# Kernel optimization log

Hardware: AMD Instinct MI355X
Metric: run time of the kernel (lower is better)

The kernel has to match this reference:

```python
import jax, jax.numpy as jnp
import numpy as np

B, C_IN, L = 4, 512, 16384
C_RED = C_IN // 2  # q/k/v reduced channels = 256
BL = 64            # sliding-window block size
NEG = -jnp.inf


def setup_inputs() -> dict:
    key = jax.random.key(0)
    ks = jax.random.split(key, 8)
    x1 = jax.random.normal(ks[0], (B, C_IN, L), dtype=jnp.float32)
    x2 = jax.random.normal(ks[1], (B, C_IN, L), dtype=jnp.float32)
    mask = jnp.ones((B, 1, L), dtype=jnp.float32)
    s = 0.02
    Wq = jax.random.normal(ks[2], (C_RED, C_IN), dtype=jnp.float32) * s
    Wk = jax.random.normal(ks[3], (C_RED, C_IN), dtype=jnp.float32) * s
    Wv = jax.random.normal(ks[4], (C_RED, C_IN), dtype=jnp.float32) * s
    Wo = jax.random.normal(ks[5], (C_IN, C_RED), dtype=jnp.float32) * s
    bq = jnp.zeros((C_RED,), jnp.float32)
    bk = jnp.zeros((C_RED,), jnp.float32)
    bv = jnp.zeros((C_RED,), jnp.float32)
    bo = jnp.zeros((C_IN,), jnp.float32)
    return {"x1": x1, "x2": x2, "mask": mask, "Wq": Wq, "bq": bq,
            "Wk": Wk, "bk": bk, "Wv": Wv, "bv": bv, "Wo": Wo, "bo": bo}


def _conv1x1(W, b, x):
    # x: (B, Cin, L) -> (B, Cout, L)
    return jnp.einsum('oc,bcl->bol', W, x) + b[None, :, None]


def reference(x1, x2, mask, Wq, bq, Wk, bk, Wv, bv, Wo, bo):
    # encoder stage: value comes from x1 (x2 unused)
    q = _conv1x1(Wq, bq, x1)  # (B, C, L)
    k = _conv1x1(Wk, bk, x1)
    v = _conv1x1(Wv, bv, x1)

    Bq, C, Lq = q.shape
    bl = BL
    nb = (Lq + bl - 1) // bl
    pad = nb * bl - Lq
    if pad > 0:
        q = jnp.pad(q, ((0, 0), (0, 0), (0, pad)))
        k = jnp.pad(k, ((0, 0), (0, 0), (0, pad)))
        v = jnp.pad(v, ((0, 0), (0, 0), (0, pad)))
        mask = jnp.pad(mask, ((0, 0), (0, 0), (0, pad)))

    # non-overlapping windows: (B, C, nb, bl)
    qb = q.reshape(Bq, C, nb, bl)
    kb = k.reshape(Bq, C, nb, bl)
    vb = v.reshape(Bq, C, nb, bl)
    mb = mask.reshape(Bq, 1, nb, bl)  # (B,1,nb,bl)

    scale = 1.0 / jnp.sqrt(jnp.float32(C))
    # per-block attention scores: (B, nb, bl_i, bl_j)
    scores = jnp.einsum('bcni,bcnj->bnij', qb, kb) * scale
    key_mask = mb[:, 0, :, None, :]  # (B, nb, 1, bl_j)
    scores = jnp.where(key_mask == 0, NEG, scores)
    probs = jax.nn.softmax(scores, axis=-1)
    attn = jnp.einsum('bnij,bcnj->bcni', probs, vb)  # (B, C, nb, bl)

    h = jax.nn.relu(attn)
    out = jnp.einsum('oc,bcni->boni', Wo, h) + bo[None, :, None, None]
    out = out.reshape(Bq, Wo.shape[0], nb * bl)
    if pad > 0:
        out = out[:, :, :Lq]
    return out
```

## Files before the change

### kernel.cpp

```cpp
#include <hip/hip_runtime.h>
#include <hip/hip_fp16.h>
#include <stdint.h>

#define BB    4
#define CIN   512
#define CRED  256
#define LL    16384
#define NBLK  256
#define WELEM 131072

typedef _Float16 half8 __attribute__((ext_vector_type(8)));
typedef float    f32x4 __attribute__((ext_vector_type(4)));

#define XT_OFF 0
#define Q_OFF  0
#define K_OFF  32768
#define V_OFF  32768
#define H_OFF  0
#define P_OFF  65536
#define MSK_OFF 73728
#define LDS_BYTES 73984

#define SWZ(r) (((r)&7)<<4)

__global__ void convert_weights(const float* __restrict__ Wq,
                                const float* __restrict__ Wk,
                                const float* __restrict__ Wv,
                                const float* __restrict__ Wo,
                                _Float16* __restrict__ dst) {
    int i = blockIdx.x * blockDim.x + threadIdx.x;
    int m = i >> 17;
    int e = i & (WELEM - 1);
    const float* src = (m == 0) ? Wq : (m == 1) ? Wk : (m == 2) ? Wv : Wo;
    dst[(size_t)m * WELEM + e] = (_Float16)src[e];
}

__global__ __launch_bounds__(256, 2)
void att_fused(const float* __restrict__ x1, const float* __restrict__ mask,
               const _Float16* __restrict__ W,
               const float* __restrict__ bq, const float* __restrict__ bk,
               const float* __restrict__ bv, const float* __restrict__ bo,
               float* __restrict__ out) {
    extern __shared__ char lds[];
    const int tid  = threadIdx.x;
    const int wid  = tid >> 6;
    const int lane = tid & 63;
    const int l15  = lane & 15;
    const int l4   = lane >> 4;
    const int blk  = blockIdx.x;
    const int b    = blk >> 8;
    const int n    = blk & 255;
    const int jx   = tid & 15;
    const int rb   = tid >> 4;

    const _Float16* Wq = W;
    const _Float16* Wk = W + WELEM;
    const _Float16* Wv = W + 2 * WELEM;
    const _Float16* Wo = W + 3 * WELEM;

    {
        const float* xbase = x1 + ((size_t)b * CIN + 2 * rb) * LL + n * 64 + 4 * jx;
        #pragma unroll
        for (int i = 0; i < 16; ++i) {
            f32x4 a = *(const f32x4*)(xbase + (size_t)(32 * i) * LL);
            f32x4 c = *(const f32x4*)(xbase + (size_t)(32 * i + 1) * LL);
            const int col = 4 * rb + 64 * i;
            #pragma unroll
            for (int u = 0; u < 4; ++u) {
                union { _Float16 h[2]; uint32_t w; } p;
                p.h[0] = (_Float16)a[u];
                p.h[1] = (_Float16)c[u];
                const int j = 4 * jx + u;
                *(uint32_t*)(lds + XT_OFF + j * 1024 + (col ^ SWZ(j))) = p.w;
            }
        }
        if (tid < 64)
            *(float*)(lds + MSK_OFF + tid * 4) = mask[(size_t)b * LL + n * 64 + tid];
    }
    __syncthreads();

    uint64_t qh[4][4], kh[4][4], vh[4][4];
    #pragma unroll
    for (int pass = 0; pass < 4; ++pass) {
        f32x4 aQ[4], aK[4], aV[4];
        #pragma unroll
        for (int q = 0; q < 4; ++q) {
            aQ[q] = (f32x4){0.f, 0.f, 0.f, 0.f};
            aK[q] = (f32x4){0.f, 0.f, 0.f, 0.f};
            aV[q] = (f32x4){0.f, 0.f, 0.f, 0.f};
        }
        const int mrow = wid * 64 + pass * 16 + l15;
        const _Float16* wqp = Wq + (size_t)mrow * CIN + l4 * 8;
        const _Float16* wkp = Wk + (size_t)mrow * CIN + l4 * 8;
        const _Float16* wvp = Wv + (size_t)mrow * CIN + l4 * 8;
        #pragma unroll 4
        for (int ks = 0; ks < 16; ++ks) {
            const int kb = ks * 64 + l4 * 16;
            half8 xb[4];
            #pragma unroll
            for (int nt = 0; nt < 4; ++nt) {
                const int j = nt * 16 + l15;
                xb[nt] = *(const half8*)(lds + XT_OFF + j * 1024 + (kb ^ SWZ(j)));
            }
            half8 aq = *(const half8*)(wqp + ks * 32);
            half8 ak = *(const half8*)(wkp + ks * 32);
            half8 av = *(const half8*)(wvp + ks * 32);
            #pragma unroll
            for (int nt = 0; nt < 4; ++nt) {
                aQ[nt] = __builtin_amdgcn_mfma_f32_16x16x32_f16(aq, xb[nt], aQ[nt], 0, 0, 0);
                aK[nt] = __builtin_amdgcn_mfma_f32_16x16x32_f16(ak, xb[nt], aK[nt], 0, 0, 0);
                aV[nt] = __builtin_amdgcn_mfma_f32_16x16x32_f16(av, xb[nt], aV[nt], 0, 0, 0);
            }
        }
        const int c0 = wid * 64 + pass * 16 + l4 * 4;
        f32x4 bqv = *(const f32x4*)(bq + c0);
        f32x4 bkv = *(const f32x4*)(bk + c0);
        f32x4 bvv = *(const f32x4*)(bv + c0);
        #pragma unroll
        for (int nt = 0; nt < 4; ++nt) {
            union { _Float16 h[4]; uint64_t q; } qp, kp, vp;
            #pragma unroll
            for (int ri = 0; ri < 4; ++ri) {
                qp.h[ri] = (_Float16)(aQ[nt][ri] + bqv[ri]);
                kp.h[ri] = (_Float16)(aK[nt][ri] + bkv[ri]);
                vp.h[ri] = (_Float16)(aV[nt][ri] + bvv[ri]);
            }
            qh[pass][nt] = qp.q;
            kh[pass][nt] = kp.q;
            vh[pass][nt] = vp.q;
        }
    }
    __syncthreads();

    #pragma unroll
    for (int pass = 0; pass < 4; ++pass) {
        const int c0 = wid * 64 + pass * 16 + l4 * 4;
        #pragma unroll
        for (int nt = 0; nt < 4; ++nt) {
            const int j = nt * 16 + l15;
            *(uint64_t*)(lds + Q_OFF + j * 512 + ((2 * c0) ^ SWZ(j))) = qh[pass][nt];
            *(uint64_t*)(lds + K_OFF + j * 512 + ((2 * c0) ^ SWZ(j))) = kh[pass][nt];
        }
    }
    __syncthreads();

    {
        const int i0 = wid * 16;
        f32x4 sa[4];
        #pragma unroll
        for (int jt = 0; jt < 4; ++jt) sa[jt] = (f32x4){0.f, 0.f, 0.f, 0.f};
        #pragma unroll
        for (int ks = 0; ks < 8; ++ks) {
            const int kb = ks * 64 + l4 * 16;
            const int iq = i0 + l15;
            half8 qa = *(const half8*)(lds + Q_OFF + iq * 512 + (kb ^ SWZ(iq)));
            #pragma unroll
            for (int jt = 0; jt < 4; ++jt) {
                const int jr = jt * 16 + l15;
                half8 kf = *(const half8*)(lds + K_OFF + jr * 512 + (kb ^ SWZ(jr)));
                sa[jt] = __builtin_amdgcn_mfma_f32_16x16x32_f16(qa, kf, sa[jt], 0, 0, 0);
            }
        }
        float msk[4];
        #pragma unroll
        for (int jt = 0; jt < 4; ++jt)
            msk[jt] = *(const float*)(lds + MSK_OFF + (jt * 16 + l15) * 4);
        #pragma unroll
        for (int ri = 0; ri < 4; ++ri) {
            float v[4];
            #pragma unroll
            for (int jt = 0; jt < 4; ++jt)
                v[jt] = (msk[jt] == 0.f) ? -1e30f : sa[jt][ri] * 0.0625f;
            float mx = fmaxf(fmaxf(v[0], v[1]), fmaxf(v[2], v[3]));
            mx = fmaxf(mx, __shfl_xor(mx, 1));
            mx = fmaxf(mx, __shfl_xor(mx, 2));
            mx = fmaxf(mx, __shfl_xor(mx, 4));
            mx = fmaxf(mx, __shfl_xor(mx, 8));
            float e[4], sum = 0.f;
            #pragma unroll
            for (int jt = 0; jt < 4; ++jt) { e[jt] = __expf(v[jt] - mx); sum += e[jt]; }
            sum += __shfl_xor(sum, 1);
            sum += __shfl_xor(sum, 2);
            sum += __shfl_xor(sum, 4);
            sum += __shfl_xor(sum, 8);
            const float inv = 1.f / sum;
            const int i = i0 + l4 * 4 + ri;
            #pragma unroll
            for (int jt = 0; jt < 4; ++jt) {
                const int j = jt * 16 + l15;
                *(_Float16*)(lds + P_OFF + i * 128 + ((2 * j) ^ SWZ(i))) =
                    (_Float16)(e[jt] * inv);
            }
        }
    }
    __syncthreads();

    #pragma unroll
    for (int pass = 0; pass < 4; ++pass) {
        const int c0 = wid * 64 + pass * 16 + l4 * 4;
        #pragma unroll
        for (int nt = 0; nt < 4; ++nt) {
            const int j = nt * 16 + l15;
            const uint64_t v64 = vh[pass][nt];
            #pragma unroll
            for (int ri = 0; ri < 4; ++ri) {
                const int c = c0 + ri;
                *(uint16_t*)(lds + V_OFF + c * 128 + ((2 * j) ^ SWZ(c))) =
                    (uint16_t)(v64 >> (16 * ri));
            }
        }
    }
    __syncthreads();

    {
        const int cb = wid * 64;
        f32x4 pv[4][4];
        #pragma unroll
        for (int m = 0; m < 4; ++m)
            #pragma unroll
            for (int q = 0; q < 4; ++q) pv[m][q] = (f32x4){0.f, 0.f, 0.f, 0.f};
        #pragma unroll
        for (int ks = 0; ks < 2; ++ks) {
            const int kb = ks * 64 + l4 * 16;
            half8 pb[4];
            #pragma unroll
            for (int nt = 0; nt < 4; ++nt) {
                const int i = nt * 16 + l15;
                pb[nt] = *(const half8*)(lds + P_OFF + i * 128 + (kb ^ SWZ(i)));
            }
            #pragma unroll
            for (int mt = 0; mt < 4; ++mt) {
                const int c = cb + mt * 16 + l15;
                half8 va = *(const half8*)(lds + V_OFF + c * 128 + (kb ^ SWZ(c)));
                #pragma unroll
                for (int nt = 0; nt < 4; ++nt)
                    pv[mt][nt] = __builtin_amdgcn_mfma_f32_16x16x32_f16(va, pb[nt], pv[mt][nt], 0, 0, 0);
            }
        }
        #pragma unroll
        for (int mt = 0; mt < 4; ++mt) {
            const int c0 = cb + mt * 16 + l4 * 4;
            #pragma unroll
            for (int nt = 0; nt < 4; ++nt) {
                const int j = nt * 16 + l15;
                union { _Float16 h[4]; uint64_t q; } hp;
                #pragma unroll
                for (int ri = 0; ri < 4; ++ri)
                    hp.h[ri] = (_Float16)fmaxf(pv[mt][nt][ri], 0.f);
                *(uint64_t*)(lds + H_OFF + j * 512 + ((2 * c0) ^ SWZ(j))) = hp.q;
            }
        }
    }
    __syncthreads();

    #pragma unroll
    for (int op = 0; op < 2; ++op) {
        const int mbo = wid * 128 + op * 64;
        const _Float16* wob = Wo + (size_t)(mbo + l15) * CRED + l4 * 8;
        f32x4 oa[4][4];
        #pragma unroll
        for (int m = 0; m < 4; ++m)
            #pragma unroll
            for (int q = 0; q < 4; ++q) oa[m][q] = (f32x4){0.f, 0.f, 0.f, 0.f};
        #pragma unroll 4
        for (int ks = 0; ks < 8; ++ks) {
            const int kb = ks * 64 + l4 * 16;
            half8 hb[4];
            #pragma unroll
            for (int nt = 0; nt < 4; ++nt) {
                const int i = nt * 16 + l15;
                hb[nt] = *(const half8*)(lds + H_OFF + i * 512 + (kb ^ SWZ(i)));
            }
            #pragma unroll
            for (int mt = 0; mt < 4; ++mt) {
                half8 wa = *(const half8*)(wob + mt * 16 * CRED + ks * 32);
                #pragma unroll
                for (int nt = 0; nt < 4; ++nt)
                    oa[mt][nt] = __builtin_amdgcn_mfma_f32_16x16x32_f16(wa, hb[nt], oa[mt][nt], 0, 0, 0);
            }
        }
        #pragma unroll
        for (int mt = 0; mt < 4; ++mt) {
            const int o0 = mbo + mt * 16 + l4 * 4;
            f32x4 bov = *(const f32x4*)(bo + o0);
            #pragma unroll
            for (int ri = 0; ri < 4; ++ri) {
                float* orow = out + ((size_t)b * CIN + (o0 + ri)) * LL + n * 64;
                #pragma unroll
                for (int nt = 0; nt < 4; ++nt)
                    orow[nt * 16 + l15] = oa[mt][nt][ri] + bov[ri];
            }
        }
    }
}

extern "C" void kernel_launch(void* const* d_in, const int* in_sizes, int n_in,
                              void* d_out, int out_size, void* d_ws, size_t ws_size,
                              hipStream_t stream) {
    const float* x1   = (const float*)d_in[0];
    const float* mask = (const float*)d_in[2];
    const float* Wq   = (const float*)d_in[3];
    const float* bq   = (const float*)d_in[4];
    const float* Wk   = (const float*)d_in[5];
    const float* bk   = (const float*)d_in[6];
    const float* Wv   = (const float*)d_in[7];
    const float* bv   = (const float*)d_in[8];
    const float* Wo   = (const float*)d_in[9];
    const float* bo   = (const float*)d_in[10];
    float* out = (float*)d_out;
    _Float16* wbuf = (_Float16*)d_ws;

    (void)hipFuncSetAttribute((const void*)att_fused,
                              hipFuncAttributeMaxDynamicSharedMemorySize, LDS_BYTES);

    convert_weights<<<2048, 256, 0, stream>>>(Wq, Wk, Wv, Wo, wbuf);
    att_fused<<<BB * NBLK, 256, LDS_BYTES, stream>>>(x1, mask, wbuf, bq, bk, bv, bo, out);
}
```

Baseline: 167.9 us.

## Hoist LDS X reads across QKV passes and vectorize x1 staging stores

The QKV projection loop is restructured so each K-step loads the four X fragments from LDS once and reuses them for all four 16-row passes. All 48 accumulators are kept live instead of 12. The x1 staging now reads 8 channel rows per thread and writes packed half8 LDS stores instead of 32-bit stores. This cuts LDS read traffic and store count, but raises VGPR/AGPR pressure a lot (192 accumulator floats), which may cause spills or lower occupancy under launch_bounds(256,2).

```diff
diff --git a/kernel.cpp b/kernel.cpp
--- a/kernel.cpp
+++ b/kernel.cpp
@@ -50,8 +50,6 @@
     const int blk  = blockIdx.x;
     const int b    = blk >> 8;
     const int n    = blk & 255;
-    const int jx   = tid & 15;
-    const int rb   = tid >> 4;
 
     const _Float16* Wq = W;
     const _Float16* Wk = W + WELEM;
@@ -59,19 +57,22 @@
     const _Float16* Wo = W + 3 * WELEM;
 
     {
-        const float* xbase = x1 + ((size_t)b * CIN + 2 * rb) * LL + n * 64 + 4 * jx;
-        #pragma unroll
-        for (int i = 0; i < 16; ++i) {
-            f32x4 a = *(const f32x4*)(xbase + (size_t)(32 * i) * LL);
-            f32x4 c = *(const f32x4*)(xbase + (size_t)(32 * i + 1) * LL);
-            const int col = 4 * rb + 64 * i;
+        const int jx = tid & 15;
+        const int rg = tid >> 4;
+        const float* xp = x1 + ((size_t)b * CIN + 8 * rg) * LL + n * 64 + 4 * jx;
+        #pragma unroll
+        for (int i = 0; i < 4; ++i) {
+            f32x4 r[8];
+            #pragma unroll
+            for (int r8 = 0; r8 < 8; ++r8)
+                r[r8] = *(const f32x4*)(xp + (size_t)(128 * i + r8) * LL);
             #pragma unroll
             for (int u = 0; u < 4; ++u) {
-                union { _Float16 h[2]; uint32_t w; } p;
-                p.h[0] = (_Float16)a[u];
-                p.h[1] = (_Float16)c[u];
                 const int j = 4 * jx + u;
-                *(uint32_t*)(lds + XT_OFF + j * 1024 + (col ^ SWZ(j))) = p.w;
+                union { _Float16 h[8]; half8 v; } pk;
+                #pragma unroll
+                for (int r8 = 0; r8 < 8; ++r8) pk.h[r8] = (_Float16)r[r8][u];
+                *(half8*)(lds + XT_OFF + j * 1024 + ((16 * rg + 256 * i) ^ SWZ(j))) = pk.v;
             }
         }
         if (tid < 64)
@@ -79,20 +80,19 @@
     }
     __syncthreads();
 
-    uint64_t qh[4][4], kh[4][4], vh[4][4];
+    f32x4 aQ[4][4], aK[4][4], aV[4][4];
     #pragma unroll
-    for (int pass = 0; pass < 4; ++pass) {
-        f32x4 aQ[4], aK[4], aV[4];
+    for (int p = 0; p < 4; ++p)
         #pragma unroll
         for (int q = 0; q < 4; ++q) {
-            aQ[q] = (f32x4){0.f, 0.f, 0.f, 0.f};
-            aK[q] = (f32x4){0.f, 0.f, 0.f, 0.f};
-            aV[q] = (f32x4){0.f, 0.f, 0.f, 0.f};
-        }
-        const int mrow = wid * 64 + pass * 16 + l15;
-        const _Float16* wqp = Wq + (size_t)mrow * CIN + l4 * 8;
-        const _Float16* wkp = Wk + (size_t)mrow * CIN + l4 * 8;
-        const _Float16* wvp = Wv + (size_t)mrow * CIN + l4 * 8;
+            aQ[p][q] = (f32x4){0.f, 0.f, 0.f, 0.f};
+            aK[p][q] = (f32x4){0.f, 0.f, 0.f, 0.f};
+            aV[p][q] = (f32x4){0.f, 0.f, 0.f, 0.f};
+        }
+    {
+        const _Float16* wq0 = Wq + (size_t)(wid * 64 + l15) * CIN + l4 * 8;
+        const _Float16* wk0 = Wk + (size_t)(wid * 64 + l15) * CIN + l4 * 8;
+        const _Float16* wv0 = Wv + (size_t)(wid * 64 + l15) * CIN + l4 * 8;
         #pragma unroll 4
         for (int ks = 0; ks < 16; ++ks) {
             const int kb = ks * 64 + l4 * 16;
@@ -102,44 +102,43 @@
                 const int j = nt * 16 + l15;
                 xb[nt] = *(const half8*)(lds + XT_OFF + j * 1024 + (kb ^ SWZ(j)));
             }
-            half8 aq = *(const half8*)(wqp + ks * 32);
-            half8 ak = *(const half8*)(wkp + ks * 32);
-            half8 av = *(const half8*)(wvp + ks * 32);
-            #pragma unroll
-            for (int nt = 0; nt < 4; ++nt) {
-                aQ[nt] = __builtin_amdgcn_mfma_f32_16x16x32_f16(aq, xb[nt], aQ[nt], 0, 0, 0);
-                aK[nt] = __builtin_amdgcn_mfma_f32_16x16x32_f16(ak, xb[nt], aK[nt], 0, 0, 0);
-                aV[nt] = __builtin_amdgcn_mfma_f32_16x16x32_f16(av, xb[nt], aV[nt], 0, 0, 0);
-            }
-        }
+            #pragma unroll
+            for (int pass = 0; pass < 4; ++pass) {
+                const size_t wo = (size_t)pass * 16 * CIN + ks * 32;
+                half8 aq = *(const half8*)(wq0 + wo);
+                half8 ak = *(const half8*)(wk0 + wo);
+                half8 av = *(const half8*)(wv0 + wo);
+                #pragma unroll
+                for (int nt = 0; nt < 4; ++nt) {
+                    aQ[pass][nt] = __builtin_amdgcn_mfma_f32_16x16x32_f16(aq, xb[nt], aQ[pass][nt], 0, 0, 0);
+                    aK[pass][nt] = __builtin_amdgcn_mfma_f32_16x16x32_f16(ak, xb[nt], aK[pass][nt], 0, 0, 0);
+                    aV[pass][nt] = __builtin_amdgcn_mfma_f32_16x16x32_f16(av, xb[nt], aV[pass][nt], 0, 0, 0);
+                }
+            }
+        }
+    }
+    __syncthreads();
+
+    uint64_t vh[4][4];
+    #pragma unroll
+    for (int pass = 0; pass < 4; ++pass) {
         const int c0 = wid * 64 + pass * 16 + l4 * 4;
         f32x4 bqv = *(const f32x4*)(bq + c0);
         f32x4 bkv = *(const f32x4*)(bk + c0);
         f32x4 bvv = *(const f32x4*)(bv + c0);
         #pragma unroll
         for (int nt = 0; nt < 4; ++nt) {
+            const int j = nt * 16 + l15;
             union { _Float16 h[4]; uint64_t q; } qp, kp, vp;
             #pragma unroll
             for (int ri = 0; ri < 4; ++ri) {
-                qp.h[ri] = (_Float16)(aQ[nt][ri] + bqv[ri]);
-                kp.h[ri] = (_Float16)(aK[nt][ri] + bkv[ri]);
-                vp.h[ri] = (_Float16)(aV[nt][ri] + bvv[ri]);
-            }
-            qh[pass][nt] = qp.q;
-            kh[pass][nt] = kp.q;
+                qp.h[ri] = (_Float16)(aQ[pass][nt][ri] + bqv[ri]);
+                kp.h[ri] = (_Float16)(aK[pass][nt][ri] + bkv[ri]);
+                vp.h[ri] = (_Float16)(aV[pass][nt][ri] + bvv[ri]);
+            }
+            *(uint64_t*)(lds + Q_OFF + j * 512 + ((2 * c0) ^ SWZ(j))) = qp.q;
+            *(uint64_t*)(lds + K_OFF + j * 512 + ((2 * c0) ^ SWZ(j))) = kp.q;
             vh[pass][nt] = vp.q;
-        }
-    }
-    __syncthreads();
-
-    #pragma unroll
-    for (int pass = 0; pass < 4; ++pass) {
-        const int c0 = wid * 64 + pass * 16 + l4 * 4;
-        #pragma unroll
-        for (int nt = 0; nt < 4; ++nt) {
-            const int j = nt * 16 + l15;
-            *(uint64_t*)(lds + Q_OFF + j * 512 + ((2 * c0) ^ SWZ(j))) = qh[pass][nt];
-            *(uint64_t*)(lds + K_OFF + j * 512 + ((2 * c0) ^ SWZ(j))) = kh[pass][nt];
         }
     }
     __syncthreads();
```

After: 291.4 us. 1.74x slower.

## Split fused attention kernel into QKV GEMM and attention/output kernels via workspace

Applied to the files above, without the earlier changes.

Replaces the single fused kernel with two kernels when the workspace is large enough. The first computes Q, K and V in fp16 and writes them to global workspace. The second reads them back and runs masked softmax, PV, ReLU and the output projection using less LDS, which allows higher occupancy (3 blocks per CU). This trades extra global traffic (about 100MB of fp16 writes and reads) for lower LDS pressure and more occupancy in each stage. The old fused kernel remains as a fallback.

```diff
diff --git a/kernel.cpp b/kernel.cpp
--- a/kernel.cpp
+++ b/kernel.cpp
@@ -12,16 +12,12 @@
 typedef _Float16 half8 __attribute__((ext_vector_type(8)));
 typedef float    f32x4 __attribute__((ext_vector_type(4)));
 
-#define XT_OFF 0
-#define Q_OFF  0
-#define K_OFF  32768
-#define V_OFF  32768
-#define H_OFF  0
-#define P_OFF  65536
-#define MSK_OFF 73728
-#define LDS_BYTES 73984
-
 #define SWZ(r) (((r)&7)<<4)
+
+#define QBASE   524288
+#define TILE_E  16384
+#define MAT_E   16777216
+#define WS_NEED ((size_t)(QBASE + 3 * MAT_E) * 2)
 
 __global__ void convert_weights(const float* __restrict__ Wq,
                                 const float* __restrict__ Wk,
@@ -34,6 +30,260 @@
     const float* src = (m == 0) ? Wq : (m == 1) ? Wk : (m == 2) ? Wv : Wo;
     dst[(size_t)m * WELEM + e] = (_Float16)src[e];
 }
+
+__global__ __launch_bounds__(256, 2)
+void qkv_gemm(const float* __restrict__ x1, const _Float16* __restrict__ W,
+              const float* __restrict__ bq, const float* __restrict__ bk,
+              const float* __restrict__ bv, _Float16* __restrict__ ws) {
+    extern __shared__ char lds[];
+    const int tid = threadIdx.x;
+    const int wid = tid >> 6;
+    const int l15 = tid & 15;
+    const int l4  = (tid & 63) >> 4;
+    const int b   = blockIdx.x >> 8;
+    const int n   = blockIdx.x & 255;
+
+    {
+        const int jx = tid & 15;
+        const int rg = tid >> 4;
+        const float* xp = x1 + ((size_t)b * CIN + 8 * rg) * LL + n * 64 + 4 * jx;
+        #pragma unroll
+        for (int i = 0; i < 4; ++i) {
+            f32x4 r[8];
+            #pragma unroll
+            for (int r8 = 0; r8 < 8; ++r8)
+                r[r8] = *(const f32x4*)(xp + (size_t)(128 * i + r8) * LL);
+            #pragma unroll
+            for (int u = 0; u < 4; ++u) {
+                const int j = 4 * jx + u;
+                union { _Float16 h[8]; half8 v; } pk;
+                #pragma unroll
+                for (int r8 = 0; r8 < 8; ++r8) pk.h[r8] = (_Float16)r[r8][u];
+                *(half8*)(lds + j * 1024 + ((16 * rg + 256 * i) ^ SWZ(j))) = pk.v;
+            }
+        }
+    }
+    __syncthreads();
+
+    const size_t t = (size_t)blockIdx.x * TILE_E;
+    #pragma unroll
+    for (int p = 0; p < 3; ++p) {
+        f32x4 am[4][4];
+        #pragma unroll
+        for (int m = 0; m < 4; ++m)
+            #pragma unroll
+            for (int q = 0; q < 4; ++q) am[m][q] = (f32x4){0.f, 0.f, 0.f, 0.f};
+        const _Float16* wp = W + (size_t)p * WELEM + (size_t)(wid * 64 + l15) * CIN + l4 * 8;
+        #pragma unroll 4
+        for (int ks = 0; ks < 16; ++ks) {
+            const int kb = ks * 64 + l4 * 16;
+            half8 xb[4];
+            #pragma unroll
+            for (int nt = 0; nt < 4; ++nt) {
+                const int j = nt * 16 + l15;
+                xb[nt] = *(const half8*)(lds + j * 1024 + (kb ^ SWZ(j)));
+            }
+            #pragma unroll
+            for (int mt = 0; mt < 4; ++mt) {
+                half8 wf = *(const half8*)(wp + mt * 16 * CIN + ks * 32);
+                #pragma unroll
+                for (int nt = 0; nt < 4; ++nt)
+                    am[mt][nt] = __builtin_amdgcn_mfma_f32_16x16x32_f16(wf, xb[nt], am[mt][nt], 0, 0, 0);
+            }
+        }
+        const float* bias = (p == 0) ? bq : (p == 1) ? bk : bv;
+        if (p < 2) {
+            _Float16* dst = ws + QBASE + (size_t)p * MAT_E + t;
+            #pragma unroll
+            for (int mt = 0; mt < 4; ++mt) {
+                const int c0 = wid * 64 + mt * 16 + l4 * 4;
+                f32x4 b4 = *(const f32x4*)(bias + c0);
+                #pragma unroll
+                for (int nt = 0; nt < 4; ++nt) {
+                    const int j = nt * 16 + l15;
+                    union { _Float16 h[4]; uint64_t q; } pk;
+                    #pragma unroll
+                    for (int ri = 0; ri < 4; ++ri)
+                        pk.h[ri] = (_Float16)(am[mt][nt][ri] + b4[ri]);
+                    *(uint64_t*)(dst + (size_t)j * 256 + c0) = pk.q;
+                }
+            }
+        } else {
+            _Float16* dst = ws + QBASE + 2 * (size_t)MAT_E + t;
+            #pragma unroll
+            for (int mt = 0; mt < 4; ++mt) {
+                const int c0 = wid * 64 + mt * 16 + l4 * 4;
+                f32x4 b4 = *(const f32x4*)(bias + c0);
+                #pragma unroll
+                for (int nt = 0; nt < 4; ++nt) {
+                    const int j = nt * 16 + l15;
+                    #pragma unroll
+                    for (int ri = 0; ri < 4; ++ri)
+                        dst[(size_t)(c0 + ri) * 64 + j] = (_Float16)(am[mt][nt][ri] + b4[ri]);
+                }
+            }
+        }
+    }
+}
+
+#define BH_OFF 0
+#define BP_OFF 32768
+#define LDS_B  40960
+
+__global__ __launch_bounds__(256, 3)
+void attn_out(const float* __restrict__ mask, const _Float16* __restrict__ ws,
+              const float* __restrict__ bo, float* __restrict__ out) {
+    extern __shared__ char lds[];
+    const int tid = threadIdx.x;
+    const int wid = tid >> 6;
+    const int l15 = tid & 15;
+    const int l4  = (tid & 63) >> 4;
+    const int b   = blockIdx.x >> 8;
+    const int n   = blockIdx.x & 255;
+
+    const size_t t = (size_t)blockIdx.x * TILE_E;
+    const _Float16* qt = ws + QBASE + t;
+    const _Float16* kt = qt + MAT_E;
+    const _Float16* vt = qt + 2 * (size_t)MAT_E;
+    const _Float16* Wo = ws + 3 * (size_t)WELEM;
+
+    {
+        const int i0 = wid * 16;
+        f32x4 sa[4];
+        #pragma unroll
+        for (int jt = 0; jt < 4; ++jt) sa[jt] = (f32x4){0.f, 0.f, 0.f, 0.f};
+        #pragma unroll
+        for (int ks = 0; ks < 8; ++ks) {
+            half8 qa = *(const half8*)(qt + (size_t)(i0 + l15) * 256 + ks * 32 + l4 * 8);
+            #pragma unroll
+            for (int jt = 0; jt < 4; ++jt) {
+                half8 kf = *(const half8*)(kt + (size_t)(jt * 16 + l15) * 256 + ks * 32 + l4 * 8);
+                sa[jt] = __builtin_amdgcn_mfma_f32_16x16x32_f16(qa, kf, sa[jt], 0, 0, 0);
+            }
+        }
+        float msk[4];
+        #pragma unroll
+        for (int jt = 0; jt < 4; ++jt)
+            msk[jt] = mask[(size_t)b * LL + n * 64 + jt * 16 + l15];
+        #pragma unroll
+        for (int ri = 0; ri < 4; ++ri) {
+            float v[4];
+            #pragma unroll
+            for (int jt = 0; jt < 4; ++jt)
+                v[jt] = (msk[jt] == 0.f) ? -1e30f : sa[jt][ri] * 0.0625f;
+            float mx = fmaxf(fmaxf(v[0], v[1]), fmaxf(v[2], v[3]));
+            mx = fmaxf(mx, __shfl_xor(mx, 1));
+            mx = fmaxf(mx, __shfl_xor(mx, 2));
+            mx = fmaxf(mx, __shfl_xor(mx, 4));
+            mx = fmaxf(mx, __shfl_xor(mx, 8));
+            float e[4], sum = 0.f;
+            #pragma unroll
+            for (int jt = 0; jt < 4; ++jt) { e[jt] = __expf(v[jt] - mx); sum += e[jt]; }
+            sum += __shfl_xor(sum, 1);
+            sum += __shfl_xor(sum, 2);
+            sum += __shfl_xor(sum, 4);
+            sum += __shfl_xor(sum, 8);
+            const float inv = 1.f / sum;
+            const int i = i0 + l4 * 4 + ri;
+            #pragma unroll
+            for (int jt = 0; jt < 4; ++jt) {
+                const int j = jt * 16 + l15;
+                *(_Float16*)(lds + BP_OFF + i * 128 + ((2 * j) ^ SWZ(i))) =
+                    (_Float16)(e[jt] * inv);
+            }
+        }
+    }
+    __syncthreads();
+
+    {
+        const int cb = wid * 64;
+        f32x4 pv[4][4];
+        #pragma unroll
+        for (int m = 0; m < 4; ++m)
+            #pragma unroll
+            for (int q = 0; q < 4; ++q) pv[m][q] = (f32x4){0.f, 0.f, 0.f, 0.f};
+        #pragma unroll
+        for (int ks = 0; ks < 2; ++ks) {
+            const int kb = ks * 64 + l4 * 16;
+            half8 pb[4];
+            #pragma unroll
+            for (int nt = 0; nt < 4; ++nt) {
+                const int i = nt * 16 + l15;
+                pb[nt] = *(const half8*)(lds + BP_OFF + i * 128 + (kb ^ SWZ(i)));
+            }
+            #pragma unroll
+            for (int mt = 0; mt < 4; ++mt) {
+                half8 va = *(const half8*)(vt + (size_t)(cb + mt * 16 + l15) * 64 + ks * 32 + l4 * 8);
+                #pragma unroll
+                for (int nt = 0; nt < 4; ++nt)
+                    pv[mt][nt] = __builtin_amdgcn_mfma_f32_16x16x32_f16(va, pb[nt], pv[mt][nt], 0, 0, 0);
+            }
+        }
+        #pragma unroll
+        for (int mt = 0; mt < 4; ++mt) {
+            const int c0 = cb + mt * 16 + l4 * 4;
+            #pragma unroll
+            for (int nt = 0; nt < 4; ++nt) {
+                const int j = nt * 16 + l15;
+                union { _Float16 h[4]; uint64_t q; } hp;
+                #pragma unroll
+                for (int ri = 0; ri < 4; ++ri)
+                    hp.h[ri] = (_Float16)fmaxf(pv[mt][nt][ri], 0.f);
+                *(uint64_t*)(lds + BH_OFF + j * 512 + ((2 * c0) ^ SWZ(j))) = hp.q;
+            }
+        }
+    }
+    __syncthreads();
+
+    #pragma unroll
+    for (int op = 0; op < 2; ++op) {
+        const int mbo = wid * 128 + op * 64;
+        const _Float16* wob = Wo + (size_t)(mbo + l15) * CRED + l4 * 8;
+        f32x4 oa[4][4];
+        #pragma unroll
+        for (int m = 0; m < 4; ++m)
+            #pragma unroll
+            for (int q = 0; q < 4; ++q) oa[m][q] = (f32x4){0.f, 0.f, 0.f, 0.f};
+        #pragma unroll 4
+        for (int ks = 0; ks < 8; ++ks) {
+            const int kb = ks * 64 + l4 * 16;
+            half8 hb[4];
+            #pragma unroll
+            for (int nt = 0; nt < 4; ++nt) {
+                const int i = nt * 16 + l15;
+                hb[nt] = *(const half8*)(lds + BH_OFF + i * 512 + (kb ^ SWZ(i)));
+            }
+            #pragma unroll
+            for (int mt = 0; mt < 4; ++mt) {
+                half8 wa = *(const half8*)(wob + mt * 16 * CRED + ks * 32);
+                #pragma unroll
+                for (int nt = 0; nt < 4; ++nt)
+                    oa[mt][nt] = __builtin_amdgcn_mfma_f32_16x16x32_f16(wa, hb[nt], oa[mt][nt], 0, 0, 0);
+            }
+        }
+        #pragma unroll
+        for (int mt = 0; mt < 4; ++mt) {
+            const int o0 = mbo + mt * 16 + l4 * 4;
+            f32x4 bov = *(const f32x4*)(bo + o0);
+            #pragma unroll
+            for (int ri = 0; ri < 4; ++ri) {
+                float* orow = out + ((size_t)b * CIN + (o0 + ri)) * LL + n * 64;
+                #pragma unroll
+                for (int nt = 0; nt < 4; ++nt)
+                    orow[nt * 16 + l15] = oa[mt][nt][ri] + bov[ri];
+            }
+        }
+    }
+}
+
+#define XT_OFF 0
+#define Q_OFF  0
+#define K_OFF  32768
+#define V_OFF  32768
+#define H_OFF  0
+#define P_OFF  65536
+#define MSK_OFF 73728
+#define LDS_BYTES 73984
 
 __global__ __launch_bounds__(256, 2)
 void att_fused(const float* __restrict__ x1, const float* __restrict__ mask,
@@ -50,8 +300,6 @@
     const int blk  = blockIdx.x;
     const int b    = blk >> 8;
     const int n    = blk & 255;
-    const int jx   = tid & 15;
-    const int rb   = tid >> 4;
 
     const _Float16* Wq = W;
     const _Float16* Wk = W + WELEM;
@@ -59,6 +307,8 @@
     const _Float16* Wo = W + 3 * WELEM;
 
     {
+        const int jx = tid & 15;
+        const int rb = tid >> 4;
         const float* xbase = x1 + ((size_t)b * CIN + 2 * rb) * LL + n * 64 + 4 * jx;
         #pragma unroll
         for (int i = 0; i < 16; ++i) {
@@ -231,7 +481,7 @@
             #pragma unroll
             for (int mt = 0; mt < 4; ++mt) {
                 const int c = cb + mt * 16 + l15;
-                half8 va = *(const half8*)(lds + V_OFF + c * 128 + (kb ^ SWZ(c)));
+                half8 va = *(const half8*)(lds + V_OFF + c * 128 + ((kb) ^ SWZ(c)));
                 #pragma unroll
                 for (int nt = 0; nt < 4; ++nt)
                     pv[mt][nt] = __builtin_amdgcn_mfma_f32_16x16x32_f16(va, pb[nt], pv[mt][nt], 0, 0, 0);
@@ -310,9 +560,16 @@
     float* out = (float*)d_out;
     _Float16* wbuf = (_Float16*)d_ws;
 
-    (void)hipFuncSetAttribute((const void*)att_fused,
-                              hipFuncAttributeMaxDynamicSharedMemorySize, LDS_BYTES);
-
     convert_weights<<<2048, 256, 0, stream>>>(Wq, Wk, Wv, Wo, wbuf);
-    att_fused<<<BB * NBLK, 256, LDS_BYTES, stream>>>(x1, mask, wbuf, bq, bk, bv, bo, out);
+
+    if (ws_size >= WS_NEED) {
+        (void)hipFuncSetAttribute((const void*)qkv_gemm,
+                                  hipFuncAttributeMaxDynamicSharedMemorySize, 65536);
+        qkv_gemm<<<BB * NBLK, 256, 65536, stream>>>(x1, wbuf, bq, bk, bv, wbuf);
+        attn_out<<<BB * NBLK, 256, LDS_B, stream>>>(mask, wbuf, bo, out);
+    } else {
+        (void)hipFuncSetAttribute((const void*)att_fused,
+                                  hipFuncAttributeMaxDynamicSharedMemorySize, LDS_BYTES);
+        att_fused<<<BB * NBLK, 256, LDS_BYTES, stream>>>(x1, mask, wbuf, bq, bk, bv, bo, out);
+    }
 }
```

After: 202.6 us. 20.7% more time.
